# Kernel optimization log

Hardware: AMD Instinct MI355X
Metric: run time of the kernel (lower is better)

The kernel has to match this reference:

```python
import jax, jax.numpy as jnp
import numpy as np

B, S, D = 16, 4096, 1024
K = 65536  # number of keys == number of concepts (identity mapping)
EPS = 1e-12


def setup_inputs() -> dict:
    key = jax.random.key(0)
    k1, k2, k3, k4, k5, k6 = jax.random.split(key, 6)
    return {
        "hidden": jax.random.normal(k1, (B, S, D), dtype=jnp.float32),
        "concept_signal": jax.random.normal(k2, (B, 1, D), dtype=jnp.float32),
        "keys": jax.random.normal(k3, (K, D), dtype=jnp.float32),
        "values": jax.random.normal(k4, (K, 1, D), dtype=jnp.float32),
        "key_to_value": jnp.arange(K, dtype=jnp.int64),
        "W_layer": jax.random.normal(k5, (D, D), dtype=jnp.float32) * 0.02,
        "b_layer": jax.random.normal(k6, (D,), dtype=jnp.float32) * 0.02,
    }


def _l2norm(x, axis=-1):
    return x / jnp.maximum(jnp.linalg.norm(x, axis=axis, keepdims=True), EPS)


def reference(hidden, concept_signal, keys, values, key_to_value, W_layer, b_layer):
    # self.layer(hidden_state): Linear(D, D)
    layer_out = jnp.einsum("bsd,ed->bse", hidden, W_layer) + b_layer  # [B, S, D]

    # Tensor branch of forward: per-sample nearest-key search.
    # q: one query position per sample (P=1) -> [B, D]
    q = concept_signal[:, 0, :]
    cos = jnp.einsum("bd,kd->bk", _l2norm(q), _l2norm(keys))  # cosine similarity [B, K]
    dist = 1.0 - cos                                           # cosine distance
    chosen_key = jnp.argmin(dist, axis=1)                      # [B] nearest key per sample
    # s = 1 - smallest_dist; with threshold=-2.0 it always passes; with
    # max_tokens_per_concept=1, k = max(1, ceil(clamp(s,0,1)*1)) == 1 token.
    concept_idx = key_to_value[chosen_key]                     # [B]
    tokens = values[concept_idx, 0, :]                         # [B, D] (first of the k=1 tokens)
    tokens = _l2norm(tokens)                                   # F.normalize(..., p=2, dim=-1)
    # vstack one token onto each sample, then stack -> [B, S+1, D]
    return jnp.concatenate([layer_out, tokens[:, None, :]], axis=1)
```

## Files before the change

### kernel.cpp

```cpp
#include <hip/hip_runtime.h>

constexpr int BB = 16;
constexpr int SS = 4096;
constexpr int DD = 1024;
constexpr int KK = 65536;
constexpr int GM = BB * SS;
constexpr int GK = DD;

typedef __attribute__((ext_vector_type(8))) short bf16x8;
typedef __attribute__((ext_vector_type(4))) float f32x4;
typedef __attribute__((ext_vector_type(8))) unsigned short ushort8;

#define GLD_LDS16(g, l)                                                        \
  __builtin_amdgcn_global_load_lds(                                            \
      (const __attribute__((address_space(1))) void*)(g),                      \
      (__attribute__((address_space(3))) void*)(l), 16, 0, 0)

__device__ __forceinline__ unsigned short f2bf(float x) {
  unsigned u = __float_as_uint(x);
  u += 0x7fffu + ((u >> 16) & 1u);
  return (unsigned short)(u >> 16);
}

__device__ __forceinline__ void cvt_body(const float* __restrict__ in,
                                         unsigned short* __restrict__ out,
                                         int i) {
  const float4* p = (const float4*)in + (size_t)i * 2;
  float4 a = p[0], b = p[1];
  ushort8 r;
  r[0] = f2bf(a.x); r[1] = f2bf(a.y); r[2] = f2bf(a.z); r[3] = f2bf(a.w);
  r[4] = f2bf(b.x); r[5] = f2bf(b.y); r[6] = f2bf(b.z); r[7] = f2bf(b.w);
  *(ushort8*)(out + (size_t)i * 8) = r;
}

__global__ void cvt_bf16(const float* __restrict__ in,
                         unsigned short* __restrict__ out, int n8) {
  int stride = gridDim.x * blockDim.x;
  for (int i = blockIdx.x * blockDim.x + threadIdx.x; i < n8; i += stride)
    cvt_body(in, out, i);
}

__global__ __launch_bounds__(256) void qsplit(const float* __restrict__ csig,
                                              unsigned short* __restrict__ qh,
                                              unsigned short* __restrict__ ql) {
  int i = blockIdx.x * 256 + threadIdx.x;
  float v = csig[i];
  unsigned short h = f2bf(v);
  float hf = __uint_as_float((unsigned)h << 16);
  qh[i] = h;
  ql[i] = f2bf(v - hf);
}

__global__ __launch_bounds__(256) void cos_mfma(
    const float* __restrict__ keys,
    const unsigned short* __restrict__ qh,
    const unsigned short* __restrict__ ql,
    float* __restrict__ pscore,
    int* __restrict__ pidx) {
  __shared__ float rs[4][16];
  __shared__ int ri[4][16];
  int tid = threadIdx.x, lane = tid & 63, w = tid >> 6;
  int fr = lane & 15, kg = lane >> 4;
  int key = blockIdx.x * 64 + w * 16 + fr;

  const float* krow = keys + (size_t)key * DD + kg * 8;
  const unsigned short* qhp = qh + fr * DD + kg * 8;
  const unsigned short* qlp = ql + fr * DD + kg * 8;

  f32x4 acc = {};
  float nrm = 0.f;

  float4 ka = *(const float4*)krow;
  float4 kb = *(const float4*)(krow + 4);
  bf16x8 h8 = *(const bf16x8*)qhp;
  bf16x8 l8 = *(const bf16x8*)qlp;

  for (int t = 0; t < 32; ++t) {
    float4 kc = ka, kd = kb;
    bf16x8 hh = h8, ll = l8;
    if (t + 1 < 32) {
      ka = *(const float4*)(krow + (t + 1) * 32);
      kb = *(const float4*)(krow + (t + 1) * 32 + 4);
      h8 = *(const bf16x8*)(qhp + (t + 1) * 32);
      l8 = *(const bf16x8*)(qlp + (t + 1) * 32);
    }
    float ke[8] = {kc.x, kc.y, kc.z, kc.w, kd.x, kd.y, kd.z, kd.w};
    ushort8 khv, klv;
#pragma unroll
    for (int j = 0; j < 8; ++j) {
      float v = ke[j];
      unsigned short h = f2bf(v);
      float hf = __uint_as_float((unsigned)h << 16);
      khv[j] = h;
      klv[j] = f2bf(v - hf);
      nrm = fmaf(v, v, nrm);
    }
    bf16x8 kh8 = *(bf16x8*)&khv, kl8 = *(bf16x8*)&klv;
    acc = __builtin_amdgcn_mfma_f32_16x16x32_bf16(hh, kh8, acc, 0, 0, 0);
    acc = __builtin_amdgcn_mfma_f32_16x16x32_bf16(ll, kh8, acc, 0, 0, 0);
    acc = __builtin_amdgcn_mfma_f32_16x16x32_bf16(hh, kl8, acc, 0, 0, 0);
  }

  nrm += __shfl_xor(nrm, 16);
  nrm += __shfl_xor(nrm, 32);
  float inv = rsqrtf(fmaxf(nrm, 1e-24f));

#pragma unroll
  for (int j = 0; j < 4; ++j) {
    float s = acc[j] * inv;
    int i = key;
#pragma unroll
    for (int off = 1; off < 16; off <<= 1) {
      float s2 = __shfl_xor(s, off);
      int i2 = __shfl_xor(i, off);
      if (s2 > s || (s2 == s && i2 < i)) { s = s2; i = i2; }
    }
    if (fr == 0) { rs[w][kg * 4 + j] = s; ri[w][kg * 4 + j] = i; }
  }
  __syncthreads();
  if (tid < 16) {
    float bs = rs[0][tid]; int bi = ri[0][tid];
#pragma unroll
    for (int w2 = 1; w2 < 4; ++w2) {
      float s = rs[w2][tid]; int i = ri[w2][tid];
      if (s > bs || (s == bs && i < bi)) { bs = s; bi = i; }
    }
    pscore[(size_t)tid * gridDim.x + blockIdx.x] = bs;
    pidx[(size_t)tid * gridDim.x + blockIdx.x] = bi;
  }
}


#define LDA8(AH, BUF) do {                                                     \
  _Pragma("unroll") for (int ms = 0; ms < 4; ++ms) {                           \
    int rowa = (wm << 7) + ((AH) << 6) + (ms << 4) + fr;                       \
    _Pragma("unroll") for (int ks = 0; ks < 2; ++ks) {                         \
      int ia = ((rowa << 6) + (ks << 5) + (kg << 3)) ^ sw;                     \
      ar[ms * 2 + ks] = *(const bf16x8*)&lds[(BUF) + ia]; } }                  \
} while (0)

#define LDB4(NP, BUF) do {                                                     \
  _Pragma("unroll") for (int nn = 0; nn < 2; ++nn) {                           \
    int rowb = (wn << 6) + ((((NP) << 1) + nn) << 4) + fr;                     \
    _Pragma("unroll") for (int ks = 0; ks < 2; ++ks) {                         \
      int ib = ((rowb << 6) + (ks << 5) + (kg << 3)) ^ sw;                     \
      br[(((NP) << 1) + nn) * 2 + ks] = *(const bf16x8*)&lds[(BUF) + ib]; } }  \
} while (0)

#define MFMAQ(AH, NP) do {                                                     \
  _Pragma("unroll") for (int ms = 0; ms < 4; ++ms)                             \
  _Pragma("unroll") for (int nn = 0; nn < 2; ++nn)                             \
  _Pragma("unroll") for (int ks = 0; ks < 2; ++ks)                             \
    acc[((AH) << 2) + ms][((NP) << 1) + nn] =                                  \
      __builtin_amdgcn_mfma_f32_16x16x32_bf16(ar[ms * 2 + ks],                 \
        br[(((NP) << 1) + nn) * 2 + ks],                                       \
        acc[((AH) << 2) + ms][((NP) << 1) + nn], 0, 0, 0);                     \
} while (0)

#define STAGEQ(GB, LB, QJ)                                                     \
  GLD_LDS16((GB) + (size_t)(((QJ) << 6) + srq) * GK + ssc,                     \
            &lds[(LB) + ((((QJ) << 9) + (wv << 6)) << 3)])

#define PH_MID do { __builtin_amdgcn_s_barrier();                              \
  asm volatile("s_waitcnt lgkmcnt(0)" ::: "memory");                           \
  __builtin_amdgcn_sched_barrier(0);                                           \
  __builtin_amdgcn_s_setprio(1); } while (0)

#define PH_END do { __builtin_amdgcn_s_setprio(0);                             \
  __builtin_amdgcn_s_barrier(); } while (0)

#define PH_END_V(N) do { __builtin_amdgcn_s_setprio(0);                        \
  asm volatile("s_waitcnt vmcnt(" #N ")" ::: "memory");                        \
  __builtin_amdgcn_sched_barrier(0);                                           \
  __builtin_amdgcn_s_barrier(); } while (0)

__global__ __launch_bounds__(512, 2) void gemm8(
    const unsigned short* __restrict__ A,
    const unsigned short* __restrict__ Bm,
    const float* __restrict__ bias,
    float* __restrict__ out) {
  __shared__ unsigned short lds[65536];

  int g = blockIdx.x;
  int t = ((g & 7) << 7) + (g >> 3);
  int mt = t >> 2, nt = t & 3;
  int m0 = mt << 8, n0 = nt << 8;

  int tid = threadIdx.x, lane = tid & 63, wv = tid >> 6;
  int wm = wv >> 2, wn = wv & 3;
  int fr = lane & 15, kg = lane >> 4;
  int sw = (fr & 7) << 3;

  int srq = (wv << 3) + (lane >> 3);
  int ssc = (((lane & 7) ^ ((lane >> 3) & 7)) << 3);

  const unsigned short* Ag = A + (size_t)m0 * GK;
  const unsigned short* Bg = Bm + (size_t)n0 * GK;

  f32x4 acc[8][4] = {};
  bf16x8 ar[8], br[8];

  {
    const unsigned short* b0 = Bg;
    const unsigned short* a1 = Ag + 64;
    const unsigned short* b1 = Bg + 64;
    STAGEQ(Ag, 0, 0); STAGEQ(Ag, 0, 1); STAGEQ(Ag, 0, 2); STAGEQ(Ag, 0, 3);
    STAGEQ(b0, 16384, 0); STAGEQ(b0, 16384, 1);
    STAGEQ(b0, 16384, 2); STAGEQ(b0, 16384, 3);
    STAGEQ(a1, 32768, 0); STAGEQ(a1, 32768, 2);
    STAGEQ(b1, 49152, 0); STAGEQ(b1, 49152, 1);
    STAGEQ(b1, 49152, 2); STAGEQ(b1, 49152, 3);
    asm volatile("s_waitcnt vmcnt(6)" ::: "memory");
    __builtin_amdgcn_sched_barrier(0);
    __builtin_amdgcn_s_barrier();
  }

  for (int i = 0; i < 7; ++i) {
    const unsigned short* a1 = Ag + (size_t)(2 * i + 1) * 64;
    const unsigned short* a2 = Ag + (size_t)(2 * i + 2) * 64;
    const unsigned short* b2 = Bg + (size_t)(2 * i + 2) * 64;
    const unsigned short* a3 = Ag + (size_t)(2 * i + 3) * 64;
    const unsigned short* b3 = Bg + (size_t)(2 * i + 3) * 64;
    LDA8(0, 0); LDB4(0, 16384);
    STAGEQ(a1, 32768, 1); STAGEQ(a1, 32768, 3);
    PH_MID; MFMAQ(0, 0); PH_END;
    LDB4(1, 16384);
    STAGEQ(a2, 0, 0); STAGEQ(a2, 0, 2);
    PH_MID; MFMAQ(0, 1); PH_END;
    LDA8(1, 0);
    STAGEQ(b2, 16384, 0); STAGEQ(b2, 16384, 1);
    PH_MID; MFMAQ(1, 0); PH_END;
    STAGEQ(b2, 16384, 2); STAGEQ(b2, 16384, 3);
    PH_MID; MFMAQ(1, 1); PH_END_V(6);
    LDA8(0, 32768); LDB4(0, 49152);
    STAGEQ(a2, 0, 1); STAGEQ(a2, 0, 3);
    PH_MID; MFMAQ(0, 0); PH_END;
    LDB4(1, 49152);
    STAGEQ(a3, 32768, 0); STAGEQ(a3, 32768, 2);
    PH_MID; MFMAQ(0, 1); PH_END;
    LDA8(1, 32768);
    STAGEQ(b3, 49152, 0); STAGEQ(b3, 49152, 1);
    PH_MID; MFMAQ(1, 0); PH_END;
    STAGEQ(b3, 49152, 2); STAGEQ(b3, 49152, 3);
    PH_MID; MFMAQ(1, 1); PH_END_V(6);
  }

  {
    const unsigned short* a15 = Ag + (size_t)15 * 64;
    LDA8(0, 0); LDB4(0, 16384);
    STAGEQ(a15, 32768, 1); STAGEQ(a15, 32768, 3);
    PH_MID; MFMAQ(0, 0); PH_END;
    LDB4(1, 16384); PH_MID; MFMAQ(0, 1); PH_END;
    LDA8(1, 0);     PH_MID; MFMAQ(1, 0); PH_END;
    PH_MID; MFMAQ(1, 1); PH_END_V(0);
    LDA8(0, 32768); LDB4(0, 49152); PH_MID; MFMAQ(0, 0); PH_END;
    LDB4(1, 49152); PH_MID; MFMAQ(0, 1); PH_END;
    LDA8(1, 32768); PH_MID; MFMAQ(1, 0); PH_END;
    PH_MID; MFMAQ(1, 1);
    __builtin_amdgcn_s_setprio(0);
  }

  int r0 = kg << 2, cc = fr;
#pragma unroll
  for (int ni = 0; ni < 4; ++ni) {
    int gcol = n0 + (wn << 6) + (ni << 4) + cc;
    float bv = bias[gcol];
#pragma unroll
    for (int mi = 0; mi < 8; ++mi) {
      int gr = m0 + (wm << 7) + (mi << 4) + r0;
#pragma unroll
      for (int j = 0; j < 4; ++j) {
        int grow = gr + j;
        size_t o = ((size_t)(grow + (grow >> 12)) << 10) + gcol;
        out[o] = acc[mi][ni][j] + bv;
      }
    }
  }
}

__global__ __launch_bounds__(256) void select_write(
    const float* __restrict__ pscore, const int* __restrict__ pidx, int nb,
    const int* __restrict__ ktv, const float* __restrict__ values,
    float* __restrict__ out) {
  __shared__ float ss[4];
  __shared__ int si[4];
  __shared__ float snrm;
  __shared__ int swin;
  int b = blockIdx.x, tid = threadIdx.x, lane = tid & 63, wv = tid >> 6;

  float best = -1e30f;
  int bidx = 0x7fffffff;
  for (int t = tid; t < nb; t += 256) {
    float s = pscore[(size_t)b * nb + t];
    int i = pidx[(size_t)b * nb + t];
    if (s > best || (s == best && i < bidx)) { best = s; bidx = i; }
  }
#pragma unroll
  for (int off = 32; off; off >>= 1) {
    float s = __shfl_xor(best, off);
    int i = __shfl_xor(bidx, off);
    if (s > best || (s == best && i < bidx)) { best = s; bidx = i; }
  }
  if (lane == 0) { ss[wv] = best; si[wv] = bidx; }
  __syncthreads();
  if (tid == 0) {
    float bs = ss[0]; int bi = si[0];
    for (int w2 = 1; w2 < 4; ++w2)
      if (ss[w2] > bs || (ss[w2] == bs && si[w2] < bi)) { bs = ss[w2]; bi = si[w2]; }
    swin = ktv[bi];
  }
  __syncthreads();
  int idx = swin;

  float4 v = ((const float4*)(values + (size_t)idx * DD))[tid];
  float nrm = v.x * v.x + v.y * v.y + v.z * v.z + v.w * v.w;
#pragma unroll
  for (int off = 32; off; off >>= 1) nrm += __shfl_xor(nrm, off);
  if (lane == 0) ss[wv] = nrm;
  __syncthreads();
  if (tid == 0) snrm = rsqrtf(fmaxf(ss[0] + ss[1] + ss[2] + ss[3], 1e-24f));
  __syncthreads();
  float inv = snrm;

  float4 o;
  o.x = v.x * inv; o.y = v.y * inv; o.z = v.z * inv; o.w = v.w * inv;
  ((float4*)(out + (((size_t)b * (SS + 1) + SS) << 10)))[tid] = o;
}

extern "C" void kernel_launch(void* const* d_in, const int* in_sizes, int n_in,
                              void* d_out, int out_size, void* d_ws,
                              size_t ws_size, hipStream_t stream) {
  const float* hidden = (const float*)d_in[0];
  const float* csig   = (const float*)d_in[1];
  const float* keys   = (const float*)d_in[2];
  const float* values = (const float*)d_in[3];
  const int*   ktv    = (const int*)d_in[4];
  const float* W      = (const float*)d_in[5];
  const float* bias   = (const float*)d_in[6];
  float* out = (float*)d_out;

  char* ws = (char*)d_ws;
  const size_t HB = (size_t)GM * GK * 2;
  const size_t WB = (size_t)DD * GK * 2;
  const size_t QB = (size_t)BB * DD * 2;
  const size_t PSB = (size_t)BB * 1024 * 4;

  unsigned short* hbf = (unsigned short*)ws;
  unsigned short* wbf = (unsigned short*)(ws + HB);
  unsigned short* qh  = (unsigned short*)(ws + HB + WB);
  unsigned short* ql  = (unsigned short*)(ws + HB + WB + QB);
  float* pscore = (float*)(ws + HB + WB + 2 * QB);
  int*   pidx   = (int*)(ws + HB + WB + 2 * QB + PSB);

  qsplit<<<64, 256, 0, stream>>>(csig, qh, ql);

  cos_mfma<<<1024, 256, 0, stream>>>(keys, qh, ql, pscore, pidx);

  cvt_bf16<<<4096, 256, 0, stream>>>(hidden, hbf, GM * GK / 8);
  cvt_bf16<<<512, 256, 0, stream>>>(W, wbf, DD * GK / 8);

  gemm8<<<1024, 512, 0, stream>>>(hbf, wbf, bias, out);

  select_write<<<BB, 256, 0, stream>>>(pscore, pidx, 1024, ktv, values, out);
}
```

Before: 379.9 us.

## Fuse key-similarity search and bf16 conversions into one interleaved prep kernel

Replaces the separate cosine-search kernel and the two fp32-to-bf16 conversion launches with one kernel. Each group of 11 blocks holds 2 similarity-search blocks and 9 conversion blocks, so the search work and the bandwidth-bound conversions run at the same time. This removes launch boundaries and the tail idle time between the three kernels. In exchange, block roles diverge, the grid mapping uses hard-coded counts, and conversion blocks may compete with the search blocks for memory bandwidth.

```diff
diff --git a/kernel.cpp b/kernel.cpp
--- a/kernel.cpp
+++ b/kernel.cpp
@@ -33,13 +33,6 @@
   *(ushort8*)(out + (size_t)i * 8) = r;
 }
 
-__global__ void cvt_bf16(const float* __restrict__ in,
-                         unsigned short* __restrict__ out, int n8) {
-  int stride = gridDim.x * blockDim.x;
-  for (int i = blockIdx.x * blockDim.x + threadIdx.x; i < n8; i += stride)
-    cvt_body(in, out, i);
-}
-
 __global__ __launch_bounds__(256) void qsplit(const float* __restrict__ csig,
                                               unsigned short* __restrict__ qh,
                                               unsigned short* __restrict__ ql) {
@@ -51,17 +44,14 @@
   ql[i] = f2bf(v - hf);
 }
 
-__global__ __launch_bounds__(256) void cos_mfma(
-    const float* __restrict__ keys,
-    const unsigned short* __restrict__ qh,
-    const unsigned short* __restrict__ ql,
-    float* __restrict__ pscore,
-    int* __restrict__ pidx) {
-  __shared__ float rs[4][16];
-  __shared__ int ri[4][16];
-  int tid = threadIdx.x, lane = tid & 63, w = tid >> 6;
+__device__ __forceinline__ void cos_mfma_body(
+    const float* __restrict__ keys, const unsigned short* __restrict__ qh,
+    const unsigned short* __restrict__ ql, float* __restrict__ pscore,
+    int* __restrict__ pidx, int cblk, int tid,
+    float (*rs)[16], int (*ri)[16]) {
+  int lane = tid & 63, w = tid >> 6;
   int fr = lane & 15, kg = lane >> 4;
-  int key = blockIdx.x * 64 + w * 16 + fr;
+  int key = cblk * 64 + w * 16 + fr;
 
   const float* krow = keys + (size_t)key * DD + kg * 8;
   const unsigned short* qhp = qh + fr * DD + kg * 8;
@@ -125,8 +115,33 @@
       float s = rs[w2][tid]; int i = ri[w2][tid];
       if (s > bs || (s == bs && i < bi)) { bs = s; bi = i; }
     }
-    pscore[(size_t)tid * gridDim.x + blockIdx.x] = bs;
-    pidx[(size_t)tid * gridDim.x + blockIdx.x] = bi;
+    pscore[(size_t)tid * 1024 + cblk] = bs;
+    pidx[(size_t)tid * 1024 + cblk] = bi;
+  }
+}
+
+__global__ __launch_bounds__(256) void fused_prep(
+    const float* __restrict__ keys, const unsigned short* __restrict__ qh,
+    const unsigned short* __restrict__ ql, float* __restrict__ pscore,
+    int* __restrict__ pidx,
+    const float* __restrict__ hidden, unsigned short* __restrict__ hbf,
+    const float* __restrict__ W, unsigned short* __restrict__ wbf) {
+  __shared__ float rs[4][16];
+  __shared__ int ri[4][16];
+  int bid = blockIdx.x, tid = threadIdx.x;
+  int g = bid / 11, r = bid - g * 11;
+  if (r < 2) {
+    cos_mfma_body(keys, qh, ql, pscore, pidx, g * 2 + r, tid, rs, ri);
+  } else {
+    int v = g * 9 + (r - 2);
+    if (v < 4096) {
+      int base = v * 256 + tid;
+#pragma unroll
+      for (int q = 0; q < 8; ++q)
+        cvt_body(hidden, hbf, base + q * (4096 * 256));
+    } else {
+      cvt_body(W, wbf, (v - 4096) * 256 + tid);
+    }
   }
 }
 
@@ -354,10 +369,8 @@
 
   qsplit<<<64, 256, 0, stream>>>(csig, qh, ql);
 
-  cos_mfma<<<1024, 256, 0, stream>>>(keys, qh, ql, pscore, pidx);
-
-  cvt_bf16<<<4096, 256, 0, stream>>>(hidden, hbf, GM * GK / 8);
-  cvt_bf16<<<512, 256, 0, stream>>>(W, wbf, DD * GK / 8);
+  fused_prep<<<5632, 256, 0, stream>>>(keys, qh, ql, pscore, pidx,
+                                       hidden, hbf, W, wbf);
 
   gemm8<<<1024, 512, 0, stream>>>(hbf, wbf, bias, out);
 
```

New measurement: 380.5 us. No clear change (+0.2%).
